# Optimization experiments

Hardware: AMD Instinct MI355X
Metric: run time of the kernel (lower is better)

## Reference

```python
import jax, jax.numpy as jnp
import numpy as np

V, D, H, L, T_BLOCK = 32000, 1024, 16, 4, 1024
HD = D // H
FF = 4 * D
EPS = 1e-5


def layer_norm(x, w, b):
    mu = jnp.mean(x, axis=-1, keepdims=True)
    var = jnp.mean(jnp.square(x - mu), axis=-1, keepdims=True)
    return (x - mu) * jax.lax.rsqrt(var + EPS) * w + b


def setup_inputs() -> dict:
    key = jax.random.key(0)
    ks = iter(jax.random.split(key, 32))
    s = 0.02
    inp = {
        "idx": jax.random.randint(next(ks), (4, 1024), 0, V, dtype=jnp.int32),
        "tok_emb": jax.random.normal(next(ks), (V, D), jnp.float32) * s,
        "pos_emb": jax.random.normal(next(ks), (T_BLOCK, D), jnp.float32) * s,
        "ln1_w": jnp.ones((L, D), jnp.float32),
        "ln1_b": jnp.zeros((L, D), jnp.float32),
        "wq": jax.random.normal(next(ks), (L, D, D), jnp.float32) * s,
        "wk": jax.random.normal(next(ks), (L, D, D), jnp.float32) * s,
        "wv": jax.random.normal(next(ks), (L, D, D), jnp.float32) * s,
        "wproj": jax.random.normal(next(ks), (L, D, D), jnp.float32) * s,
        "bproj": jnp.zeros((L, D), jnp.float32),
        "ln2_w": jnp.ones((L, D), jnp.float32),
        "ln2_b": jnp.zeros((L, D), jnp.float32),
        "w1": jax.random.normal(next(ks), (L, D, FF), jnp.float32) * s,
        "b1": jnp.zeros((L, FF), jnp.float32),
        "w2": jax.random.normal(next(ks), (L, FF, D), jnp.float32) * s,
        "b2": jnp.zeros((L, D), jnp.float32),
        "lnf_w": jnp.ones((D,), jnp.float32),
        "lnf_b": jnp.zeros((D,), jnp.float32),
        "wout": jax.random.normal(next(ks), (D, V), jnp.float32) * s,
        "bout": jnp.zeros((V,), jnp.float32),
    }
    return inp


def reference(idx, tok_emb, pos_emb, ln1_w, ln1_b, wq, wk, wv, wproj, bproj,
              ln2_w, ln2_b, w1, b1, w2, b2, lnf_w, lnf_b, wout, bout):
    B, T = idx.shape
    x = tok_emb[idx] + pos_emb[:T]  # (B,T,D)
    causal = jnp.tril(jnp.ones((T, T), bool))
    scale = 1.0 / jnp.sqrt(jnp.asarray(HD, x.dtype))
    for l in range(L):
        h = layer_norm(x, ln1_w[l], ln1_b[l])
        q = (h @ wq[l]).reshape(B, T, H, HD)
        k = (h @ wk[l]).reshape(B, T, H, HD)
        v = (h @ wv[l]).reshape(B, T, H, HD)
        scores = jnp.einsum('bqhd,bkhd->bhqk', q, k) * scale
        scores = jnp.where(causal, scores, -jnp.inf)
        weights = jax.nn.softmax(scores, axis=-1)
        attn = jnp.einsum('bhqk,bkhd->bqhd', weights, v).reshape(B, T, D)
        x = x + attn @ wproj[l] + bproj[l]
        h2 = layer_norm(x, ln2_w[l], ln2_b[l])
        x = x + jax.nn.relu(h2 @ w1[l] + b1[l]) @ w2[l] + b2[l]
    x = layer_norm(x, lnf_w, lnf_b)
    logits = x @ wout + bout  # (B,T,V)
    return logits
```

## Files before the change

### kernel.cpp

```cpp
#include <hip/hip_runtime.h>
#include <hip/hip_bf16.h>

#define V_  32000
#define D_  1024
#define H_  16
#define L_  4
#define T_  1024
#define B_  4
#define HD_ 64
#define FF_ 4096
#define M_  4096
#define QP_ 3072

typedef unsigned short u16;
typedef float  f32x4   __attribute__((ext_vector_type(4)));
typedef float  f32x16  __attribute__((ext_vector_type(16)));
typedef __bf16 bf16x8  __attribute__((ext_vector_type(8)));
typedef u16    us8     __attribute__((ext_vector_type(8)));

typedef __attribute__((address_space(1))) void gvoid;
typedef __attribute__((address_space(3))) void lvoid;

__device__ __forceinline__ void glds16(const void* g, void* l) {
  __builtin_amdgcn_global_load_lds((gvoid*)g, (lvoid*)l, 16, 0, 0);
}
__device__ __forceinline__ u16 f2bf(float f) {
  __hip_bfloat16 h = __float2bfloat16(f);
  return reinterpret_cast<u16&>(h);
}

__global__ __launch_bounds__(256) void embed_kernel(
    const int* __restrict__ idx, const float* __restrict__ tok,
    const float* __restrict__ pos, float* __restrict__ x)
{
  int bt = blockIdx.x;
  int t  = bt & (T_ - 1);
  int id = idx[bt];
  float4 a = ((const float4*)(tok + (size_t)id * D_))[threadIdx.x];
  float4 p = ((const float4*)(pos + (size_t)t  * D_))[threadIdx.x];
  a.x += p.x; a.y += p.y; a.z += p.z; a.w += p.w;
  ((float4*)(x + (size_t)bt * D_))[threadIdx.x] = a;
}

__global__ __launch_bounds__(256) void ln_kernel(
    const float* __restrict__ x, const float* __restrict__ w,
    const float* __restrict__ b, u16* __restrict__ out)
{
  int row = blockIdx.x;
  float4 v = ((const float4*)(x + (size_t)row * D_))[threadIdx.x];
  float s  = v.x + v.y + v.z + v.w;
  float s2 = v.x * v.x + v.y * v.y + v.z * v.z + v.w * v.w;
#pragma unroll
  for (int m = 1; m < 64; m <<= 1) { s += __shfl_xor(s, m); s2 += __shfl_xor(s2, m); }
  __shared__ float ssum[4], ssum2[4];
  int wv = threadIdx.x >> 6;
  if ((threadIdx.x & 63) == 0) { ssum[wv] = s; ssum2[wv] = s2; }
  __syncthreads();
  s  = ssum[0]  + ssum[1]  + ssum[2]  + ssum[3];
  s2 = ssum2[0] + ssum2[1] + ssum2[2] + ssum2[3];
  float mu  = s * (1.f / D_);
  float var = s2 * (1.f / D_) - mu * mu;
  float rs  = rsqrtf(var + 1e-5f);
  float4 wv4 = ((const float4*)w)[threadIdx.x];
  float4 bv4 = ((const float4*)b)[threadIdx.x];
  u16* o = out + (size_t)row * D_ + threadIdx.x * 4;
  o[0] = f2bf((v.x - mu) * rs * wv4.x + bv4.x);
  o[1] = f2bf((v.y - mu) * rs * wv4.y + bv4.y);
  o[2] = f2bf((v.z - mu) * rs * wv4.z + bv4.z);
  o[3] = f2bf((v.w - mu) * rs * wv4.w + bv4.w);
}

__global__ __launch_bounds__(256) void transpose_convert(
    const float* __restrict__ in, u16* __restrict__ out, int R, int C,
    size_t inStride, size_t outStride)
{
  __shared__ float tile[32][33];
  in  += (size_t)blockIdx.z * inStride;
  out += (size_t)blockIdx.z * outStride;
  int c  = blockIdx.x * 32 + threadIdx.x;
  int r0 = blockIdx.y * 32;
#pragma unroll
  for (int j = 0; j < 4; j++)
    tile[threadIdx.y + 8 * j][threadIdx.x] =
        in[(size_t)(r0 + threadIdx.y + 8 * j) * C + c];
  __syncthreads();
  int rr = r0 + threadIdx.x;
  int cb = blockIdx.x * 32;
#pragma unroll
  for (int j = 0; j < 4; j++)
    out[(size_t)(cb + threadIdx.y + 8 * j) * R + rr] =
        f2bf(tile[threadIdx.x][threadIdx.y + 8 * j]);
}

template<int EPI>
__global__ __launch_bounds__(256) void gemm_bt(
    const u16* __restrict__ A, const u16* __restrict__ Bt,
    const float* __restrict__ bias, const float* __restrict__ resid,
    void* __restrict__ Cout, int M, int N, int K)
{
  __shared__ u16 As[128 * 32];
  __shared__ u16 Bs[128 * 32];
  const int tid = threadIdx.x;
  const int m0 = blockIdx.x * 128;
  const int n0 = blockIdx.y * 128;
  const int w = tid >> 6, lane = tid & 63, lg = lane >> 4, lr = lane & 15;
  const int wr = w >> 1, wc = w & 1;
  f32x4 acc[4][4] = {};
  const int srow = tid >> 2;
  const int scol = (tid & 3) << 3;
  const u16* ap = A  + (size_t)(m0 + srow) * K + scol;
  const u16* bp = Bt + (size_t)(n0 + srow) * K + scol;
  u16* alds  = &As[tid * 8];
  u16* alds2 = &As[2048 + tid * 8];
  u16* blds  = &Bs[tid * 8];
  u16* blds2 = &Bs[2048 + tid * 8];
  for (int k0 = 0; k0 < K; k0 += 32) {
    __syncthreads();
    glds16(ap + k0,                  alds);
    glds16(ap + (size_t)64 * K + k0, alds2);
    glds16(bp + k0,                  blds);
    glds16(bp + (size_t)64 * K + k0, blds2);
    __syncthreads();
    bf16x8 af[4], bfr[4];
#pragma unroll
    for (int i = 0; i < 4; i++)
      af[i] = *(const bf16x8*)&As[(wr * 64 + i * 16 + lr) * 32 + lg * 8];
#pragma unroll
    for (int j = 0; j < 4; j++)
      bfr[j] = *(const bf16x8*)&Bs[(wc * 64 + j * 16 + lr) * 32 + lg * 8];
#pragma unroll
    for (int i = 0; i < 4; i++)
#pragma unroll
      for (int j = 0; j < 4; j++)
        acc[i][j] = __builtin_amdgcn_mfma_f32_16x16x32_bf16(af[i], bfr[j], acc[i][j], 0, 0, 0);
  }
#pragma unroll
  for (int i = 0; i < 4; i++) {
#pragma unroll
    for (int j = 0; j < 4; j++) {
      int col = n0 + wc * 64 + j * 16 + lr;
      float bv = bias ? bias[col] : 0.f;
#pragma unroll
      for (int r = 0; r < 4; r++) {
        int row = m0 + wr * 64 + i * 16 + lg * 4 + r;
        float val = acc[i][j][r] + bv;
        size_t o = (size_t)row * N + col;
        if (EPI == 0)      ((u16*)Cout)[o]   = f2bf(val);
        else if (EPI == 1) ((u16*)Cout)[o]   = f2bf(val > 0.f ? val : 0.f);
        else if (EPI == 2) ((float*)Cout)[o] = resid[o] + val;
        else               ((float*)Cout)[o] = val;
      }
    }
  }
}

#define BAR() __builtin_amdgcn_s_barrier()
#define LGKM0() do { asm volatile("s_waitcnt lgkmcnt(0)" ::: "memory"); \
                     __builtin_amdgcn_sched_barrier(0); } while (0)
#define VMC(n) asm volatile("s_waitcnt vmcnt(" #n ")" ::: "memory")

#define MQ(MS, NS) do { \
  _Pragma("unroll") for (int mq_ = 0; mq_ < 2; ++mq_) \
  _Pragma("unroll") for (int kq_ = 0; kq_ < 4; ++kq_) \
    acc[(MS)+mq_][NS] = __builtin_amdgcn_mfma_f32_32x32x16_bf16( \
        af[mq_][kq_], bfv[NS][kq_], acc[(MS)+mq_][NS], 0, 0, 0); \
  } while (0)

#define KTILE(BB, TT) do { \
  const int t_ = (TT); \
  const bool sn_ = (t_ + 1 < NT), sn2_ = (t_ + 2 < NT); \
  if (sn_) { stA((BB) ^ 1, t_ + 1, 1); stB((BB) ^ 1, t_ + 1, 0); stB((BB) ^ 1, t_ + 1, 1); } \
  _Pragma("unroll") for (int mi_ = 0; mi_ < 2; ++mi_) \
  _Pragma("unroll") for (int kq_ = 0; kq_ < 4; ++kq_) af[mi_][kq_] = ldA(BB, mi_, kq_); \
  _Pragma("unroll") for (int kq_ = 0; kq_ < 4; ++kq_) bfv[0][kq_] = ldB(BB, 0, kq_); \
  BAR(); LGKM0(); \
  __builtin_amdgcn_s_setprio(1); MQ(0, 0); __builtin_amdgcn_s_setprio(0); BAR(); \
  _Pragma("unroll") for (int kq_ = 0; kq_ < 4; ++kq_) bfv[1][kq_] = ldB(BB, 1, kq_); \
  BAR(); LGKM0(); \
  __builtin_amdgcn_s_setprio(1); MQ(0, 1); __builtin_amdgcn_s_setprio(0); BAR(); \
  _Pragma("unroll") for (int mi_ = 0; mi_ < 2; ++mi_) \
  _Pragma("unroll") for (int kq_ = 0; kq_ < 4; ++kq_) af[mi_][kq_] = ldA(BB, 2 + mi_, kq_); \
  BAR(); LGKM0(); \
  __builtin_amdgcn_s_setprio(1); MQ(2, 0); __builtin_amdgcn_s_setprio(0); BAR(); \
  if (sn2_) { stA((BB), t_ + 2, 0); VMC(2); } else { VMC(0); } \
  BAR(); \
  __builtin_amdgcn_s_setprio(1); MQ(2, 1); __builtin_amdgcn_s_setprio(0); BAR(); \
} while (0)

template<int EPI>
__global__ __launch_bounds__(512, 2) void gemm256(
    const u16* __restrict__ A, const u16* __restrict__ Bt,
    const float* __restrict__ bias, void* __restrict__ Cout, int N, int K)
{
  extern __shared__ char smem[];
  const int tid = threadIdx.x;
  const int nwg = gridDim.x;
  const int orig = blockIdx.x;
  const int qq = nwg >> 3, rr = nwg & 7, xcd = orig & 7, lid = orig >> 3;
  const int swz = (xcd < rr ? xcd * (qq + 1) : rr * (qq + 1) + (xcd - rr) * qq) + lid;
  const int m0 = (swz & 15) << 8;
  const int n0 = (swz >> 4) << 8;
  const int NT = K >> 6;

  const int wid = tid >> 6, lane = tid & 63;
  const int wr = wid >> 2, wc = wid & 3;
  const int l31 = lane & 31, lh = lane >> 5;
  const int gsw = (lane & 7) ^ ((lane >> 3) & 3);
  const int srow = tid >> 3, sslot = tid & 7;
  const int sg = (srow & 7) ^ ((srow >> 3) & 3);
  const int scol = ((sslot ^ sg) << 3);
  const u16* Ag = A  + (size_t)(m0 + srow) * K + scol;
  const u16* Bg = Bt + (size_t)(n0 + srow) * K + scol;
  char* ldst = smem + tid * 16;

  auto stA = [&](int bb, int kt, int h) {
    const u16* g = Ag + (size_t)(h << 7) * K + (kt << 6);
    char* l = ldst + bb * 65536 + h * 16384;
    glds16(g, l);
    glds16(g + ((size_t)K << 6), l + 8192);
  };
  auto stB = [&](int bb, int kt, int h) {
    const u16* g = Bg + (size_t)(h << 7) * K + (kt << 6);
    char* l = ldst + bb * 65536 + 32768 + h * 16384;
    glds16(g, l);
    glds16(g + ((size_t)K << 6), l + 8192);
  };
  auto ldA = [&](int bb, int mf, int ks) {
    return *(const bf16x8*)(smem + bb * 65536 +
        ((wr * 128 + mf * 32 + l31) << 7) + (((ks * 2 + lh) ^ gsw) << 4));
  };
  auto ldB = [&](int bb, int nf, int ks) {
    return *(const bf16x8*)(smem + bb * 65536 + 32768 +
        ((wc * 64 + nf * 32 + l31) << 7) + (((ks * 2 + lh) ^ gsw) << 4));
  };

  f32x16 acc[4][2] = {};
  bf16x8 af[2][4], bfv[2][4];

  stA(0, 0, 0); stA(0, 0, 1); stB(0, 0, 0); stB(0, 0, 1);
  stA(1, 1, 0);
  VMC(2); BAR();

  for (int t = 0; t < NT; t += 2) {
    KTILE(0, t);
    KTILE(1, t + 1);
  }

#pragma unroll
  for (int nf = 0; nf < 2; ++nf) {
    const int col = n0 + wc * 64 + nf * 32 + l31;
    const float bv = bias ? bias[col] : 0.f;
#pragma unroll
    for (int mf = 0; mf < 4; ++mf) {
#pragma unroll
      for (int v = 0; v < 16; ++v) {
        const int row = m0 + wr * 128 + mf * 32 + (v & 3) + 8 * (v >> 2) + 4 * lh;
        float val = acc[mf][nf][v] + bv;
        size_t o = (size_t)row * N + col;
        if (EPI == 0)      ((u16*)Cout)[o]   = f2bf(val);
        else if (EPI == 1) ((u16*)Cout)[o]   = f2bf(val > 0.f ? val : 0.f);
        else               ((float*)Cout)[o] = val;
      }
    }
  }
}

__global__ __launch_bounds__(512) void attn_kernel(
    const u16* __restrict__ qkv, u16* __restrict__ o)
{
  __shared__ u16 Ks[64][72];
  __shared__ u16 Vt[64][72];
  __shared__ u16 Ps[8][16][72];
  const int qt = blockIdx.x;
  const int bh = blockIdx.y;
  const int b = bh >> 4, h = bh & 15;
  const int tid = threadIdx.x;
  const int w = tid >> 6, lane = tid & 63, lg = lane >> 4, lr = lane & 15;
  const int q0 = qt * 128;
  const size_t qbase = ((size_t)b * T_) * QP_ + h * HD_;
  const size_t obase = ((size_t)b * T_) * D_ + h * HD_;
  const u16* qb = qkv + qbase;
  const u16* kb = qkv + qbase + D_;
  const u16* vb = qkv + qbase + 2 * D_;
  bf16x8 qf[2];
  const int qrow = q0 + w * 16 + lr;
#pragma unroll
  for (int ks = 0; ks < 2; ks++)
    qf[ks] = *(const bf16x8*)&qb[(size_t)qrow * QP_ + ks * 32 + lg * 8];
  f32x4 oacc[4] = {};
  float mrun[4] = {-1e30f, -1e30f, -1e30f, -1e30f};
  float lrun[4] = {0.f, 0.f, 0.f, 0.f};
  const int srow = tid >> 3;
  const int scol = (tid & 7) << 3;
  const int ktmax = 2 * qt + 1;
  us8 kv = *(const us8*)&kb[(size_t)srow * QP_ + scol];
  us8 vv = *(const us8*)&vb[(size_t)srow * QP_ + scol];
  for (int kt = 0; kt <= ktmax; kt++) {
    __syncthreads();
    *(us8*)&Ks[srow][scol] = kv;
#pragma unroll
    for (int jj = 0; jj < 8; jj++) Vt[scol + jj][srow] = vv[jj];
    __syncthreads();
    if (kt < ktmax) {
      kv = *(const us8*)&kb[(size_t)((kt + 1) * 64 + srow) * QP_ + scol];
      vv = *(const us8*)&vb[(size_t)((kt + 1) * 64 + srow) * QP_ + scol];
    }
    f32x4 s[4] = {};
#pragma unroll
    for (int ks = 0; ks < 2; ks++)
#pragma unroll
      for (int j = 0; j < 4; j++) {
        bf16x8 kf = *(const bf16x8*)&Ks[j * 16 + lr][ks * 32 + lg * 8];
        s[j] = __builtin_amdgcn_mfma_f32_16x16x32_bf16(qf[ks], kf, s[j], 0, 0, 0);
      }
#pragma unroll
    for (int j = 0; j < 4; j++) {
      int key = kt * 64 + j * 16 + lr;
#pragma unroll
      for (int r = 0; r < 4; r++) {
        int qr = q0 + w * 16 + lg * 4 + r;
        s[j][r] = (key <= qr) ? s[j][r] * 0.125f : -1e30f;
      }
    }
    float al[4];
#pragma unroll
    for (int r = 0; r < 4; r++) {
      float t0 = fmaxf(fmaxf(s[0][r], s[1][r]), fmaxf(s[2][r], s[3][r]));
#pragma unroll
      for (int m = 1; m < 16; m <<= 1) t0 = fmaxf(t0, __shfl_xor(t0, m));
      float mnew = fmaxf(mrun[r], t0);
      al[r] = __expf(mrun[r] - mnew);
      mrun[r] = mnew;
    }
#pragma unroll
    for (int j = 0; j < 4; j++)
#pragma unroll
      for (int r = 0; r < 4; r++)
        s[j][r] = __expf(s[j][r] - mrun[r]);
#pragma unroll
    for (int r = 0; r < 4; r++) {
      float rs = s[0][r] + s[1][r] + s[2][r] + s[3][r];
#pragma unroll
      for (int m = 1; m < 16; m <<= 1) rs += __shfl_xor(rs, m);
      lrun[r] = lrun[r] * al[r] + rs;
#pragma unroll
      for (int jd = 0; jd < 4; jd++) oacc[jd][r] *= al[r];
    }
#pragma unroll
    for (int j = 0; j < 4; j++)
#pragma unroll
      for (int r = 0; r < 4; r++)
        Ps[w][lg * 4 + r][j * 16 + lr] = f2bf(s[j][r]);
    asm volatile("s_waitcnt lgkmcnt(0)" ::: "memory");
    __builtin_amdgcn_sched_barrier(0);
#pragma unroll
    for (int ks = 0; ks < 2; ks++) {
      bf16x8 pf = *(const bf16x8*)&Ps[w][lr][ks * 32 + lg * 8];
#pragma unroll
      for (int jd = 0; jd < 4; jd++) {
        bf16x8 vf = *(const bf16x8*)&Vt[jd * 16 + lr][ks * 32 + lg * 8];
        oacc[jd] = __builtin_amdgcn_mfma_f32_16x16x32_bf16(pf, vf, oacc[jd], 0, 0, 0);
      }
    }
  }
#pragma unroll
  for (int jd = 0; jd < 4; jd++)
#pragma unroll
    for (int r = 0; r < 4; r++) {
      int row = q0 + w * 16 + lg * 4 + r;
      o[obase + (size_t)row * D_ + jd * 16 + lr] = f2bf(oacc[jd][r] / lrun[r]);
    }
}

extern "C" void kernel_launch(void* const* d_in, const int* in_sizes, int n_in,
                              void* d_out, int out_size, void* d_ws, size_t ws_size,
                              hipStream_t stream)
{
  const int*   idx   = (const int*)  d_in[0];
  const float* tok   = (const float*)d_in[1];
  const float* pos   = (const float*)d_in[2];
  const float* ln1w  = (const float*)d_in[3];
  const float* ln1b  = (const float*)d_in[4];
  const float* wq    = (const float*)d_in[5];
  const float* wk    = (const float*)d_in[6];
  const float* wvw   = (const float*)d_in[7];
  const float* wproj = (const float*)d_in[8];
  const float* bproj = (const float*)d_in[9];
  const float* ln2w  = (const float*)d_in[10];
  const float* ln2b  = (const float*)d_in[11];
  const float* w1    = (const float*)d_in[12];
  const float* b1    = (const float*)d_in[13];
  const float* w2    = (const float*)d_in[14];
  const float* b2    = (const float*)d_in[15];
  const float* lnfw  = (const float*)d_in[16];
  const float* lnfb  = (const float*)d_in[17];
  const float* wout  = (const float*)d_in[18];
  const float* bout  = (const float*)d_in[19];

  hipFuncSetAttribute(reinterpret_cast<const void*>(&gemm256<0>),
                      hipFuncAttributeMaxDynamicSharedMemorySize, 131072);
  hipFuncSetAttribute(reinterpret_cast<const void*>(&gemm256<1>),
                      hipFuncAttributeMaxDynamicSharedMemorySize, 131072);
  hipFuncSetAttribute(reinterpret_cast<const void*>(&gemm256<3>),
                      hipFuncAttributeMaxDynamicSharedMemorySize, 131072);

  char* ws = (char*)d_ws;
  size_t off = 0;
  auto alloc = [&](size_t bytes) {
    void* p = ws + off;
    off += (bytes + 255) & ~(size_t)255;
    return p;
  };
  u16* wqkvT  = (u16*)alloc((size_t)L_ * 3 * D_ * D_ * 2);
  u16* wprojT = (u16*)alloc((size_t)L_ * D_ * D_ * 2);
  u16* w1T    = (u16*)alloc((size_t)L_ * D_ * FF_ * 2);
  u16* w2T    = (u16*)alloc((size_t)L_ * D_ * FF_ * 2);
  u16* woutT  = (u16*)alloc((size_t)D_ * V_ * 2);
  float* x    = (float*)alloc((size_t)M_ * D_ * 4);
  u16* hbuf   = (u16*)alloc((size_t)M_ * D_ * 2);
  u16* qkvbuf = (u16*)alloc((size_t)M_ * QP_ * 2);
  u16* abuf   = (u16*)alloc((size_t)M_ * D_ * 2);
  u16* f1buf  = (u16*)alloc((size_t)M_ * FF_ * 2);

  dim3 tb(32, 8);
  const size_t DD = (size_t)D_ * D_, DF = (size_t)D_ * FF_;
  transpose_convert<<<dim3(D_ / 32, D_ / 32, L_), tb, 0, stream>>>(wq,    wqkvT,          D_,  D_, DD, 3 * DD);
  transpose_convert<<<dim3(D_ / 32, D_ / 32, L_), tb, 0, stream>>>(wk,    wqkvT + DD,     D_,  D_, DD, 3 * DD);
  transpose_convert<<<dim3(D_ / 32, D_ / 32, L_), tb, 0, stream>>>(wvw,   wqkvT + 2 * DD, D_,  D_, DD, 3 * DD);
  transpose_convert<<<dim3(D_ / 32, D_ / 32, L_), tb, 0, stream>>>(wproj, wprojT,         D_,  D_, DD, DD);
  transpose_convert<<<dim3(FF_ / 32, D_ / 32, L_), tb, 0, stream>>>(w1,   w1T,            D_,  FF_, DF, DF);
  transpose_convert<<<dim3(D_ / 32, FF_ / 32, L_), tb, 0, stream>>>(w2,   w2T,            FF_, D_, DF, DF);
  transpose_convert<<<dim3(V_ / 32, D_ / 32, 1),  tb, 0, stream>>>(wout,  woutT,          D_,  V_, 0, 0);

  embed_kernel<<<M_, 256, 0, stream>>>(idx, tok, pos, x);

  dim3 gD(M_ / 128, D_ / 128);
  for (int l = 0; l < L_; l++) {
    size_t wo = (size_t)l * DD;
    size_t fo = (size_t)l * DF;
    ln_kernel<<<M_, 256, 0, stream>>>(x, ln1w + l * D_, ln1b + l * D_, hbuf);
    gemm256<0><<<dim3(16 * (QP_ / 256)), 512, 131072, stream>>>(
        hbuf, wqkvT + (size_t)l * 3 * DD, nullptr, qkvbuf, QP_, D_);
    attn_kernel<<<dim3(T_ / 128, B_ * H_), 512, 0, stream>>>(qkvbuf, abuf);
    gemm_bt<2><<<gD, 256, 0, stream>>>(abuf, wprojT + wo, bproj + l * D_, x, x, M_, D_, D_);
    ln_kernel<<<M_, 256, 0, stream>>>(x, ln2w + l * D_, ln2b + l * D_, hbuf);
    gemm256<1><<<dim3(16 * (FF_ / 256)), 512, 131072, stream>>>(
        hbuf, w1T + fo, b1 + l * FF_, f1buf, FF_, D_);
    gemm_bt<2><<<gD, 256, 0, stream>>>(f1buf, w2T + fo, b2 + l * D_, x, x, M_, D_, FF_);
  }
  ln_kernel<<<M_, 256, 0, stream>>>(x, lnfw, lnfb, hbuf);
  gemm256<3><<<dim3(16 * (V_ / 256)), 512, 131072, stream>>>(
      hbuf, woutT, bout, d_out, V_, D_);
}
```

Baseline: 1.647 ms.

## Restructure GEMM main loop into register double-buffered MFMA clusters with fewer barriers

Replaces the two-tile unrolled K loop with a per-tile loop that issues all global-to-LDS loads for the next tile up front. LDS fragment reads are split into half-K register buffers so the next fragments load while the current MFMA cluster runs, using partial lgkmcnt waits. This removes most intra-tile barriers. In exchange it waits for vmcnt(0) plus a barrier at the end of every tile, so there is less prefetch depth than the old staggered A-load scheme. It also uses more registers for the fragment buffers.

```diff
diff --git a/kernel.cpp b/kernel.cpp
--- a/kernel.cpp
+++ b/kernel.cpp
@@ -155,36 +155,18 @@
 }
 
 #define BAR() __builtin_amdgcn_s_barrier()
-#define LGKM0() do { asm volatile("s_waitcnt lgkmcnt(0)" ::: "memory"); \
-                     __builtin_amdgcn_sched_barrier(0); } while (0)
 #define VMC(n) asm volatile("s_waitcnt vmcnt(" #n ")" ::: "memory")
-
-#define MQ(MS, NS) do { \
+#define LGKMC(n) do { asm volatile("s_waitcnt lgkmcnt(" #n ")" ::: "memory"); \
+                      __builtin_amdgcn_sched_barrier(0); } while (0)
+
+#define CLUSTER(AF, BV, MS) do { \
+  __builtin_amdgcn_s_setprio(1); \
   _Pragma("unroll") for (int mq_ = 0; mq_ < 2; ++mq_) \
-  _Pragma("unroll") for (int kq_ = 0; kq_ < 4; ++kq_) \
-    acc[(MS)+mq_][NS] = __builtin_amdgcn_mfma_f32_32x32x16_bf16( \
-        af[mq_][kq_], bfv[NS][kq_], acc[(MS)+mq_][NS], 0, 0, 0); \
-  } while (0)
-
-#define KTILE(BB, TT) do { \
-  const int t_ = (TT); \
-  const bool sn_ = (t_ + 1 < NT), sn2_ = (t_ + 2 < NT); \
-  if (sn_) { stA((BB) ^ 1, t_ + 1, 1); stB((BB) ^ 1, t_ + 1, 0); stB((BB) ^ 1, t_ + 1, 1); } \
-  _Pragma("unroll") for (int mi_ = 0; mi_ < 2; ++mi_) \
-  _Pragma("unroll") for (int kq_ = 0; kq_ < 4; ++kq_) af[mi_][kq_] = ldA(BB, mi_, kq_); \
-  _Pragma("unroll") for (int kq_ = 0; kq_ < 4; ++kq_) bfv[0][kq_] = ldB(BB, 0, kq_); \
-  BAR(); LGKM0(); \
-  __builtin_amdgcn_s_setprio(1); MQ(0, 0); __builtin_amdgcn_s_setprio(0); BAR(); \
-  _Pragma("unroll") for (int kq_ = 0; kq_ < 4; ++kq_) bfv[1][kq_] = ldB(BB, 1, kq_); \
-  BAR(); LGKM0(); \
-  __builtin_amdgcn_s_setprio(1); MQ(0, 1); __builtin_amdgcn_s_setprio(0); BAR(); \
-  _Pragma("unroll") for (int mi_ = 0; mi_ < 2; ++mi_) \
-  _Pragma("unroll") for (int kq_ = 0; kq_ < 4; ++kq_) af[mi_][kq_] = ldA(BB, 2 + mi_, kq_); \
-  BAR(); LGKM0(); \
-  __builtin_amdgcn_s_setprio(1); MQ(2, 0); __builtin_amdgcn_s_setprio(0); BAR(); \
-  if (sn2_) { stA((BB), t_ + 2, 0); VMC(2); } else { VMC(0); } \
-  BAR(); \
-  __builtin_amdgcn_s_setprio(1); MQ(2, 1); __builtin_amdgcn_s_setprio(0); BAR(); \
+  _Pragma("unroll") for (int nq_ = 0; nq_ < 2; ++nq_) \
+  _Pragma("unroll") for (int kq_ = 0; kq_ < 2; ++kq_) \
+    acc[(MS)+mq_][nq_] = __builtin_amdgcn_mfma_f32_32x32x16_bf16( \
+        AF[mq_][kq_], BV[nq_][kq_], acc[(MS)+mq_][nq_], 0, 0, 0); \
+  __builtin_amdgcn_s_setprio(0); \
 } while (0)
 
 template<int EPI>
@@ -235,15 +217,39 @@
   };
 
   f32x16 acc[4][2] = {};
-  bf16x8 af[2][4], bfv[2][4];
+  bf16x8 afA[2][2], afB[2][2], bfvA[2][2], bfvB[2][2];
 
   stA(0, 0, 0); stA(0, 0, 1); stB(0, 0, 0); stB(0, 0, 1);
-  stA(1, 1, 0);
-  VMC(2); BAR();
-
-  for (int t = 0; t < NT; t += 2) {
-    KTILE(0, t);
-    KTILE(1, t + 1);
+  VMC(0); BAR();
+
+  for (int t = 0; t < NT; ++t) {
+    const int bb = t & 1;
+    if (t + 1 < NT) {
+      stA(bb ^ 1, t + 1, 0); stA(bb ^ 1, t + 1, 1);
+      stB(bb ^ 1, t + 1, 0); stB(bb ^ 1, t + 1, 1);
+    }
+#pragma unroll
+    for (int i = 0; i < 2; i++) {
+      afA[i][0]  = ldA(bb, i, 0);     afA[i][1]  = ldA(bb, i, 1);
+      bfvA[i][0] = ldB(bb, i, 0);     bfvA[i][1] = ldB(bb, i, 1);
+    }
+#pragma unroll
+    for (int i = 0; i < 2; i++) { afB[i][0] = ldA(bb, 2 + i, 0); afB[i][1] = ldA(bb, 2 + i, 1); }
+    LGKMC(4);
+    CLUSTER(afA, bfvA, 0);
+#pragma unroll
+    for (int i = 0; i < 2; i++) { bfvB[i][0] = ldB(bb, i, 2); bfvB[i][1] = ldB(bb, i, 3); }
+#pragma unroll
+    for (int i = 0; i < 2; i++) { afA[i][0] = ldA(bb, i, 2); afA[i][1] = ldA(bb, i, 3); }
+    LGKMC(8);
+    CLUSTER(afB, bfvA, 2);
+#pragma unroll
+    for (int i = 0; i < 2; i++) { afB[i][0] = ldA(bb, 2 + i, 2); afB[i][1] = ldA(bb, 2 + i, 3); }
+    LGKMC(4);
+    CLUSTER(afA, bfvB, 0);
+    LGKMC(0);
+    CLUSTER(afB, bfvB, 2);
+    VMC(0); BAR();
   }
 
 #pragma unroll
```

New measurement: 1.643 ms. About the same (-0.2%).
